# Kernel optimization log

Hardware: AMD Instinct MI355X
Metric: run time of the kernel (lower is better)

The kernel has to match this reference:

```python
import jax, jax.numpy as jnp
import numpy as np

N_NODES = 100000
N_EDGES = 1280000
IN_DIM = 64
OUT_DIM = 64


def setup_inputs() -> dict:
    key = jax.random.key(0)
    k1, k2, k3, k4, k5 = jax.random.split(key, 5)
    features = jax.random.normal(k1, (N_NODES, IN_DIM), dtype=jnp.float32)
    w = jax.random.uniform(k2, (N_EDGES,), dtype=jnp.float32)
    # torch nn.Linear weight is [out, in]; we store it as [in, out] so h @ W
    W = jax.random.normal(k3, (IN_DIM, OUT_DIM), dtype=jnp.float32) * (1.0 / np.sqrt(IN_DIM))
    src = jax.random.randint(k4, (N_EDGES,), 0, N_NODES, dtype=jnp.int64 if jax.config.jax_enable_x64 else jnp.int32)
    dst = jax.random.randint(k5, (N_EDGES,), 0, N_NODES, dtype=jnp.int64 if jax.config.jax_enable_x64 else jnp.int32)
    return {"features": features, "w": w, "W": W, "src": src, "dst": dst}


def reference(features, w, W, src, dst):
    num_nodes = features.shape[0]
    # u_mul_e: per-edge message = h[src] * w  (edge-weighted SpMM gather-multiply)
    msg = features[src] * w[:, None]                     # [E, in_dim]
    # fn.sum('m','h'): scatter-add messages to destination nodes
    agg = jax.ops.segment_sum(msg, dst, num_segments=num_nodes)  # [N, in_dim]
    # D_in = 1 / clamp(in_degree, min=1)
    deg = jax.ops.segment_sum(jnp.ones_like(w), dst, num_segments=num_nodes)
    d_in = 1.0 / jnp.maximum(deg, 1.0)                   # [N]
    h = agg * d_in[:, None]
    # linear (bias=False), activation None, batch_norm False, dropout 0
    return h @ W                                         # [N, out_dim]
```

## Files before the change

kernel.cpp:

```cpp
#include <hip/hip_runtime.h>

#define N_NODES 100000
#define N_EDGES 1280000
#define DIM 64
#define NBINS 391
#define CAP 3712
#define EPB 4096
#define NFB 313
#define CONVB 512
#define NTILES 1563
#define FPAD 68
#define WSCALE (1.0f / 32767.0f)

__device__ __forceinline__ unsigned bf16_rne(float x) {
    unsigned u = __float_as_uint(x);
    return (u + 0x7fffu + ((u >> 16) & 1u)) >> 16;
}
__device__ __forceinline__ float bf_lo(unsigned q) { return __uint_as_float(q << 16); }
__device__ __forceinline__ float bf_hi(unsigned q) { return __uint_as_float(q & 0xffff0000u); }

__global__ __launch_bounds__(256) void k_fill_conv(
    const int* __restrict__ src, const float* __restrict__ w,
    const int* __restrict__ dst, int* __restrict__ cursor,
    uint2* __restrict__ binned,
    const float* __restrict__ feat, const float* __restrict__ W,
    unsigned short* __restrict__ fW) {
    __shared__ union U {
        struct { int h[NBINS]; int base_[NBINS]; } fill;
        struct { float w[DIM * DIM]; float f[64 * FPAD]; } conv;
        __device__ U() {}
    } sm;
    int t = threadIdx.x;

    if (blockIdx.x < NFB) {
        for (int i = t; i < NBINS; i += 256) sm.fill.h[i] = 0;
        __syncthreads();
        int eb = blockIdx.x * EPB;
        int d[16], sv[16];
        unsigned wq[16];
        #pragma unroll
        for (int j = 0; j < 16; ++j) {
            int e = eb + j * 256 + t;
            if (e < N_EDGES) {
                d[j] = dst[e];
                sv[j] = src[e];
                wq[j] = (unsigned)(w[e] * 32767.0f + 0.5f);
                atomicAdd(&sm.fill.h[d[j] >> 8], 1);
            } else d[j] = -1;
        }
        __syncthreads();
        for (int i = t; i < NBINS; i += 256) {
            int c = sm.fill.h[i];
            sm.fill.base_[i] = c ? atomicAdd(&cursor[i], c) : 0;
            sm.fill.h[i] = 0;
        }
        __syncthreads();
        #pragma unroll
        for (int j = 0; j < 16; ++j) {
            if (d[j] >= 0) {
                int bin = d[j] >> 8;
                int pos = sm.fill.base_[bin] + atomicAdd(&sm.fill.h[bin], 1);
                binned[bin * CAP + pos] =
                    make_uint2((unsigned)sv[j] | ((unsigned)(d[j] & 255) << 17), wq[j]);
            }
        }
    } else {
        #pragma unroll
        for (int i = 0; i < DIM * DIM / 256; ++i)
            sm.conv.w[t + i * 256] = W[t + i * 256];
        const float4* lds_w4 = (const float4*)sm.conv.w;
        float4* lds_f4 = (float4*)sm.conv.f;
        int tx = t & 15, ny = t >> 4;
        int rr = t >> 2, seg = t & 3;

        for (int tb = blockIdx.x - NFB; tb < NTILES; tb += CONVB) {
            int nb = tb * 64;
            __syncthreads();
            #pragma unroll
            for (int q = 0; q < 4; ++q) {
                float4 v = (nb + rr < N_NODES)
                           ? ((const float4*)feat)[(size_t)(nb + rr) * 16 + seg * 4 + q]
                           : make_float4(0.f, 0.f, 0.f, 0.f);
                lds_f4[(rr * FPAD + seg * 16 + q * 4) >> 2] = v;
            }
            __syncthreads();
            float acc[4][4];
            #pragma unroll
            for (int i = 0; i < 4; ++i)
                #pragma unroll
                for (int j = 0; j < 4; ++j) acc[i][j] = 0.f;
            for (int k0 = 0; k0 < DIM; k0 += 4) {
                float4 hv[4], wv[4];
                #pragma unroll
                for (int i = 0; i < 4; ++i)
                    hv[i] = lds_f4[((ny * 4 + i) * FPAD + k0) >> 2];
                #pragma unroll
                for (int j = 0; j < 4; ++j)
                    wv[j] = lds_w4[((k0 + j) * DIM + tx * 4) >> 2];
                #pragma unroll
                for (int i = 0; i < 4; ++i) {
                    const float* hp = (const float*)&hv[i];
                    #pragma unroll
                    for (int kk = 0; kk < 4; ++kk) {
                        float hk = hp[kk];
                        acc[i][0] = fmaf(hk, ((const float*)&wv[kk])[0], acc[i][0]);
                        acc[i][1] = fmaf(hk, ((const float*)&wv[kk])[1], acc[i][1]);
                        acc[i][2] = fmaf(hk, ((const float*)&wv[kk])[2], acc[i][2]);
                        acc[i][3] = fmaf(hk, ((const float*)&wv[kk])[3], acc[i][3]);
                    }
                }
            }
            #pragma unroll
            for (int i = 0; i < 4; ++i) {
                int node = nb + ny * 4 + i;
                if (node < N_NODES) {
                    ushort4 o;
                    o.x = (unsigned short)bf16_rne(acc[i][0]);
                    o.y = (unsigned short)bf16_rne(acc[i][1]);
                    o.z = (unsigned short)bf16_rne(acc[i][2]);
                    o.w = (unsigned short)bf16_rne(acc[i][3]);
                    *(ushort4*)(fW + (size_t)node * DIM + tx * 4) = o;
                }
            }
        }
    }
}

__global__ __launch_bounds__(512) void k_sortbin(const uint2* __restrict__ binned,
                                                 const int* __restrict__ cursor,
                                                 unsigned* __restrict__ csrp,
                                                 int* __restrict__ offs,
                                                 int* __restrict__ cnt) {
    __shared__ int h[256];
    __shared__ int excl[256];
    __shared__ unsigned stage[CAP];
    int b = blockIdx.x, t = threadIdx.x;
    int total = cursor[b];
    int segbase = b * CAP;
    if (t < 256) h[t] = 0;
    __syncthreads();
    for (int i = t; i < total; i += 512)
        atomicAdd(&h[(binned[segbase + i].x >> 17) & 255], 1);
    __syncthreads();
    int v = 0;
    if (t < 256) { v = h[t]; excl[t] = v; }
    __syncthreads();
    for (int off = 1; off < 256; off <<= 1) {
        int add = 0;
        if (t < 256 && t >= off) add = excl[t - off];
        __syncthreads();
        if (t < 256) excl[t] += add;
        __syncthreads();
    }
    if (t < 256) {
        int ex = excl[t] - v;
        excl[t] = ex;
        int node = (b << 8) + t;
        if (node < N_NODES) { cnt[node] = v; offs[node] = segbase + ex; }
        h[t] = 0;
    }
    __syncthreads();
    for (int i = t; i < total; i += 512) {
        uint2 e = binned[segbase + i];
        int o = (e.x >> 17) & 255;
        int pos = excl[o] + atomicAdd(&h[o], 1);
        if (pos < CAP) stage[pos] = (e.x & 0x1ffffu) | (e.y << 17);
    }
    __syncthreads();
    for (int i = t; i < total; i += 512)
        csrp[segbase + i] = stage[i];
}

__global__ __launch_bounds__(256) void k_gather(const uint4* __restrict__ fW4,
                                                const unsigned* __restrict__ csrp,
                                                const int* __restrict__ offs,
                                                const int* __restrict__ cnt,
                                                float* __restrict__ out) {
    int lane = threadIdx.x & 63;
    int g = lane >> 3, s = lane & 7;
    int wave = (blockIdx.x * 256 + threadIdx.x) >> 6;
    int nw = gridDim.x * 4;

    for (int node = wave; node < N_NODES; node += nw) {
        int start = offs[node];
        int c = cnt[node];
        int end = start + c;
        float a[8] = {0, 0, 0, 0, 0, 0, 0, 0};
        for (int i = start; i < end; i += 32) {
            int i0 = i + g, i1 = i + 8 + g, i2 = i + 16 + g, i3 = i + 24 + g;
            unsigned p0 = csrp[(i0 < end) ? i0 : start];
            unsigned p1 = csrp[(i1 < end) ? i1 : start];
            unsigned p2 = csrp[(i2 < end) ? i2 : start];
            unsigned p3 = csrp[(i3 < end) ? i3 : start];
            float w0 = (i0 < end) ? (float)(p0 >> 17) * WSCALE : 0.f;
            float w1 = (i1 < end) ? (float)(p1 >> 17) * WSCALE : 0.f;
            float w2 = (i2 < end) ? (float)(p2 >> 17) * WSCALE : 0.f;
            float w3 = (i3 < end) ? (float)(p3 >> 17) * WSCALE : 0.f;
            uint4 q0 = fW4[((p0 & 0x1ffffu) << 3) + s];
            uint4 q1 = fW4[((p1 & 0x1ffffu) << 3) + s];
            uint4 q2 = fW4[((p2 & 0x1ffffu) << 3) + s];
            uint4 q3 = fW4[((p3 & 0x1ffffu) << 3) + s];
            a[0] = fmaf(bf_lo(q0.x), w0, a[0]); a[1] = fmaf(bf_hi(q0.x), w0, a[1]);
            a[2] = fmaf(bf_lo(q0.y), w0, a[2]); a[3] = fmaf(bf_hi(q0.y), w0, a[3]);
            a[4] = fmaf(bf_lo(q0.z), w0, a[4]); a[5] = fmaf(bf_hi(q0.z), w0, a[5]);
            a[6] = fmaf(bf_lo(q0.w), w0, a[6]); a[7] = fmaf(bf_hi(q0.w), w0, a[7]);
            a[0] = fmaf(bf_lo(q1.x), w1, a[0]); a[1] = fmaf(bf_hi(q1.x), w1, a[1]);
            a[2] = fmaf(bf_lo(q1.y), w1, a[2]); a[3] = fmaf(bf_hi(q1.y), w1, a[3]);
            a[4] = fmaf(bf_lo(q1.z), w1, a[4]); a[5] = fmaf(bf_hi(q1.z), w1, a[5]);
            a[6] = fmaf(bf_lo(q1.w), w1, a[6]); a[7] = fmaf(bf_hi(q1.w), w1, a[7]);
            a[0] = fmaf(bf_lo(q2.x), w2, a[0]); a[1] = fmaf(bf_hi(q2.x), w2, a[1]);
            a[2] = fmaf(bf_lo(q2.y), w2, a[2]); a[3] = fmaf(bf_hi(q2.y), w2, a[3]);
            a[4] = fmaf(bf_lo(q2.z), w2, a[4]); a[5] = fmaf(bf_hi(q2.z), w2, a[5]);
            a[6] = fmaf(bf_lo(q2.w), w2, a[6]); a[7] = fmaf(bf_hi(q2.w), w2, a[7]);
            a[0] = fmaf(bf_lo(q3.x), w3, a[0]); a[1] = fmaf(bf_hi(q3.x), w3, a[1]);
            a[2] = fmaf(bf_lo(q3.y), w3, a[2]); a[3] = fmaf(bf_hi(q3.y), w3, a[3]);
            a[4] = fmaf(bf_lo(q3.z), w3, a[4]); a[5] = fmaf(bf_hi(q3.z), w3, a[5]);
            a[6] = fmaf(bf_lo(q3.w), w3, a[6]); a[7] = fmaf(bf_hi(q3.w), w3, a[7]);
        }
        #pragma unroll
        for (int j = 0; j < 8; ++j) {
            a[j] += __shfl_xor(a[j], 8, 64);
            a[j] += __shfl_xor(a[j], 16, 64);
            a[j] += __shfl_xor(a[j], 32, 64);
        }
        float dinv = 1.0f / fmaxf((float)c, 1.0f);
        if (g == 0) {
            float4 o0, o1;
            o0.x = a[0] * dinv; o0.y = a[1] * dinv; o0.z = a[2] * dinv; o0.w = a[3] * dinv;
            o1.x = a[4] * dinv; o1.y = a[5] * dinv; o1.z = a[6] * dinv; o1.w = a[7] * dinv;
            ((float4*)out)[node * 16 + s * 2 + 0] = o0;
            ((float4*)out)[node * 16 + s * 2 + 1] = o1;
        }
    }
}

extern "C" void kernel_launch(void* const* d_in, const int* in_sizes, int n_in,
                              void* d_out, int out_size, void* d_ws, size_t ws_size,
                              hipStream_t stream) {
    const float* feat = (const float*)d_in[0];
    const float* w    = (const float*)d_in[1];
    const float* W    = (const float*)d_in[2];
    const int*   src  = (const int*)d_in[3];
    const int*   dst  = (const int*)d_in[4];
    float* out = (float*)d_out;

    unsigned short* fW = (unsigned short*)d_ws;
    uint2* binned  = (uint2*)(fW + (size_t)N_NODES * DIM);
    unsigned* csrp = (unsigned*)(binned + (size_t)NBINS * CAP);
    int* offs      = (int*)(csrp + (size_t)NBINS * CAP);
    int* cnt       = offs + N_NODES;
    int* cursor    = cnt + N_NODES;

    hipMemsetAsync(cursor, 0, NBINS * sizeof(int), stream);

    k_fill_conv<<<NFB + CONVB, 256, 0, stream>>>(src, w, dst, cursor, binned,
                                                 feat, W, fW);
    k_sortbin<<<NBINS, 512, 0, stream>>>(binned, cursor, csrp, offs, cnt);
    k_gather<<<4096, 256, 0, stream>>>((const uint4*)fW, csrp, offs, cnt, out);
}
```

Measured before the change: 151.4 us.

## Fuse bin sort and gather into one kernel using LDS-staged CSR

Merges the per-bin counting sort and the gather/aggregate pass into one kernel. Each block sorts its bin's edges into shared memory and then gathers directly from that staged CSR, which removes the global csrp/offs/cnt round trip and one launch. Bins shrink from 256 to 128 nodes so a bin fits in LDS and in four edges per thread, and outputs use nontemporal stores. The trade-offs are less gather parallelism per block (8 waves over 128 nodes) and a hard capacity assumption of at most 4 edges per thread and CAP edges per bin.

```diff
diff --git a/kernel.cpp b/kernel.cpp
--- a/kernel.cpp
+++ b/kernel.cpp
@@ -3,14 +3,17 @@
 #define N_NODES 100000
 #define N_EDGES 1280000
 #define DIM 64
-#define NBINS 391
-#define CAP 3712
+#define NBINS 782
+#define BINN 128
+#define CAP 1984
 #define EPB 4096
 #define NFB 313
 #define CONVB 512
 #define NTILES 1563
 #define FPAD 68
 #define WSCALE (1.0f / 32767.0f)
+
+typedef float floatx4 __attribute__((ext_vector_type(4)));
 
 __device__ __forceinline__ unsigned bf16_rne(float x) {
     unsigned u = __float_as_uint(x);
@@ -45,7 +48,7 @@
                 d[j] = dst[e];
                 sv[j] = src[e];
                 wq[j] = (unsigned)(w[e] * 32767.0f + 0.5f);
-                atomicAdd(&sm.fill.h[d[j] >> 8], 1);
+                atomicAdd(&sm.fill.h[d[j] >> 7], 1);
             } else d[j] = -1;
         }
         __syncthreads();
@@ -58,10 +61,10 @@
         #pragma unroll
         for (int j = 0; j < 16; ++j) {
             if (d[j] >= 0) {
-                int bin = d[j] >> 8;
+                int bin = d[j] >> 7;
                 int pos = sm.fill.base_[bin] + atomicAdd(&sm.fill.h[bin], 1);
                 binned[bin * CAP + pos] =
-                    make_uint2((unsigned)sv[j] | ((unsigned)(d[j] & 255) << 17), wq[j]);
+                    make_uint2((unsigned)sv[j] | ((unsigned)(d[j] & 127) << 17), wq[j]);
             }
         }
     } else {
@@ -126,80 +129,75 @@
     }
 }
 
-__global__ __launch_bounds__(512) void k_sortbin(const uint2* __restrict__ binned,
-                                                 const int* __restrict__ cursor,
-                                                 unsigned* __restrict__ csrp,
-                                                 int* __restrict__ offs,
-                                                 int* __restrict__ cnt) {
-    __shared__ int h[256];
-    __shared__ int excl[256];
+__global__ __launch_bounds__(512) void k_sortgather(
+    const uint2* __restrict__ binned, const int* __restrict__ cursor,
+    const uint4* __restrict__ fW4, float* __restrict__ out) {
     __shared__ unsigned stage[CAP];
-    int b = blockIdx.x, t = threadIdx.x;
+    __shared__ int hist[BINN];
+    __shared__ int excl[BINN];
+    __shared__ int hcur[BINN];
+    int t = threadIdx.x, b = blockIdx.x;
     int total = cursor[b];
-    int segbase = b * CAP;
-    if (t < 256) h[t] = 0;
-    __syncthreads();
-    for (int i = t; i < total; i += 512)
-        atomicAdd(&h[(binned[segbase + i].x >> 17) & 255], 1);
+    const uint2* eb = binned + (size_t)b * CAP;
+    if (t < BINN) { hist[t] = 0; hcur[t] = 0; }
+    __syncthreads();
+
+    uint2 ed[4];
+    int ne = 0;
+    for (int i = t; i < total; i += 512) {
+        ed[ne] = eb[i];
+        atomicAdd(&hist[(ed[ne].x >> 17) & 127], 1);
+        ++ne;
+    }
     __syncthreads();
     int v = 0;
-    if (t < 256) { v = h[t]; excl[t] = v; }
-    __syncthreads();
-    for (int off = 1; off < 256; off <<= 1) {
+    if (t < BINN) { v = hist[t]; excl[t] = v; }
+    __syncthreads();
+    #pragma unroll
+    for (int off = 1; off < BINN; off <<= 1) {
         int add = 0;
-        if (t < 256 && t >= off) add = excl[t - off];
-        __syncthreads();
-        if (t < 256) excl[t] += add;
-        __syncthreads();
-    }
-    if (t < 256) {
-        int ex = excl[t] - v;
-        excl[t] = ex;
-        int node = (b << 8) + t;
-        if (node < N_NODES) { cnt[node] = v; offs[node] = segbase + ex; }
-        h[t] = 0;
-    }
-    __syncthreads();
-    for (int i = t; i < total; i += 512) {
-        uint2 e = binned[segbase + i];
-        int o = (e.x >> 17) & 255;
-        int pos = excl[o] + atomicAdd(&h[o], 1);
-        if (pos < CAP) stage[pos] = (e.x & 0x1ffffu) | (e.y << 17);
-    }
-    __syncthreads();
-    for (int i = t; i < total; i += 512)
-        csrp[segbase + i] = stage[i];
-}
-
-__global__ __launch_bounds__(256) void k_gather(const uint4* __restrict__ fW4,
-                                                const unsigned* __restrict__ csrp,
-                                                const int* __restrict__ offs,
-                                                const int* __restrict__ cnt,
-                                                float* __restrict__ out) {
-    int lane = threadIdx.x & 63;
+        if (t < BINN && t >= off) add = excl[t - off];
+        __syncthreads();
+        if (t < BINN) excl[t] += add;
+        __syncthreads();
+    }
+    if (t < BINN) excl[t] -= v;
+    __syncthreads();
+    #pragma unroll
+    for (int k = 0; k < 4; ++k) {
+        if (k < ne) {
+            unsigned x = ed[k].x;
+            int o = (x >> 17) & 127;
+            int pos = excl[o] + atomicAdd(&hcur[o], 1);
+            stage[pos] = (x & 0x1ffffu) | (ed[k].y << 17);
+        }
+    }
+    __syncthreads();
+
+    int lane = t & 63;
+    int wv = t >> 6;
     int g = lane >> 3, s = lane & 7;
-    int wave = (blockIdx.x * 256 + threadIdx.x) >> 6;
-    int nw = gridDim.x * 4;
-
-    for (int node = wave; node < N_NODES; node += nw) {
-        int start = offs[node];
-        int c = cnt[node];
+    for (int n = wv; n < BINN; n += 8) {
+        int node = (b << 7) + n;
+        if (node >= N_NODES) break;
+        int start = excl[n];
+        int c = hist[n];
         int end = start + c;
         float a[8] = {0, 0, 0, 0, 0, 0, 0, 0};
         for (int i = start; i < end; i += 32) {
             int i0 = i + g, i1 = i + 8 + g, i2 = i + 16 + g, i3 = i + 24 + g;
-            unsigned p0 = csrp[(i0 < end) ? i0 : start];
-            unsigned p1 = csrp[(i1 < end) ? i1 : start];
-            unsigned p2 = csrp[(i2 < end) ? i2 : start];
-            unsigned p3 = csrp[(i3 < end) ? i3 : start];
+            unsigned p0 = stage[(i0 < end) ? i0 : start];
+            unsigned p1 = stage[(i1 < end) ? i1 : start];
+            unsigned p2 = stage[(i2 < end) ? i2 : start];
+            unsigned p3 = stage[(i3 < end) ? i3 : start];
             float w0 = (i0 < end) ? (float)(p0 >> 17) * WSCALE : 0.f;
             float w1 = (i1 < end) ? (float)(p1 >> 17) * WSCALE : 0.f;
             float w2 = (i2 < end) ? (float)(p2 >> 17) * WSCALE : 0.f;
             float w3 = (i3 < end) ? (float)(p3 >> 17) * WSCALE : 0.f;
-            uint4 q0 = fW4[((p0 & 0x1ffffu) << 3) + s];
-            uint4 q1 = fW4[((p1 & 0x1ffffu) << 3) + s];
-            uint4 q2 = fW4[((p2 & 0x1ffffu) << 3) + s];
-            uint4 q3 = fW4[((p3 & 0x1ffffu) << 3) + s];
+            uint4 q0 = fW4[((size_t)(p0 & 0x1ffffu) << 3) + s];
+            uint4 q1 = fW4[((size_t)(p1 & 0x1ffffu) << 3) + s];
+            uint4 q2 = fW4[((size_t)(p2 & 0x1ffffu) << 3) + s];
+            uint4 q3 = fW4[((size_t)(p3 & 0x1ffffu) << 3) + s];
             a[0] = fmaf(bf_lo(q0.x), w0, a[0]); a[1] = fmaf(bf_hi(q0.x), w0, a[1]);
             a[2] = fmaf(bf_lo(q0.y), w0, a[2]); a[3] = fmaf(bf_hi(q0.y), w0, a[3]);
             a[4] = fmaf(bf_lo(q0.z), w0, a[4]); a[5] = fmaf(bf_hi(q0.z), w0, a[5]);
@@ -225,11 +223,12 @@
         }
         float dinv = 1.0f / fmaxf((float)c, 1.0f);
         if (g == 0) {
-            float4 o0, o1;
+            floatx4 o0, o1;
             o0.x = a[0] * dinv; o0.y = a[1] * dinv; o0.z = a[2] * dinv; o0.w = a[3] * dinv;
             o1.x = a[4] * dinv; o1.y = a[5] * dinv; o1.z = a[6] * dinv; o1.w = a[7] * dinv;
-            ((float4*)out)[node * 16 + s * 2 + 0] = o0;
-            ((float4*)out)[node * 16 + s * 2 + 1] = o1;
+            floatx4* op = (floatx4*)out + (size_t)node * 16 + s * 2;
+            __builtin_nontemporal_store(o0, op + 0);
+            __builtin_nontemporal_store(o1, op + 1);
         }
     }
 }
@@ -246,15 +245,11 @@
 
     unsigned short* fW = (unsigned short*)d_ws;
     uint2* binned  = (uint2*)(fW + (size_t)N_NODES * DIM);
-    unsigned* csrp = (unsigned*)(binned + (size_t)NBINS * CAP);
-    int* offs      = (int*)(csrp + (size_t)NBINS * CAP);
-    int* cnt       = offs + N_NODES;
-    int* cursor    = cnt + N_NODES;
+    int* cursor    = (int*)(binned + (size_t)NBINS * CAP);
 
     hipMemsetAsync(cursor, 0, NBINS * sizeof(int), stream);
 
     k_fill_conv<<<NFB + CONVB, 256, 0, stream>>>(src, w, dst, cursor, binned,
                                                  feat, W, fW);
-    k_sortbin<<<NBINS, 512, 0, stream>>>(binned, cursor, csrp, offs, cnt);
-    k_gather<<<4096, 256, 0, stream>>>((const uint4*)fW, csrp, offs, cnt, out);
-}
+    k_sortgather<<<NBINS, 512, 0, stream>>>(binned, cursor, (const uint4*)fW, out);
+}
```

New measurement: 182.8 us. 1.21x slower.

## Process two nodes per wavefront in gather, pack offset/count, use nontemporal loads/stores

Applied to the files above, without the earlier changes.

The gather kernel now gives each half-wave (32 lanes) its own destination node, so one wave handles two nodes at once and walks 16 edges per iteration instead of 32. This cuts the lanes idling on masked edges for low-degree nodes (average degree about 13) and drops one shuffle-reduction stage. Offsets and counts are packed into a single int2 array, so each node needs one load instead of two. Edge-list reads and output writes use nontemporal hints to keep them from polluting the cache used for feature rows. As a side effect, per-node loop trip counts can now diverge between the two halves of a wave.

```diff
diff --git a/kernel.cpp b/kernel.cpp
--- a/kernel.cpp
+++ b/kernel.cpp
@@ -11,6 +11,8 @@
 #define NTILES 1563
 #define FPAD 68
 #define WSCALE (1.0f / 32767.0f)
+
+typedef float floatx4 __attribute__((ext_vector_type(4)));
 
 __device__ __forceinline__ unsigned bf16_rne(float x) {
     unsigned u = __float_as_uint(x);
@@ -129,8 +131,7 @@
 __global__ __launch_bounds__(512) void k_sortbin(const uint2* __restrict__ binned,
                                                  const int* __restrict__ cursor,
                                                  unsigned* __restrict__ csrp,
-                                                 int* __restrict__ offs,
-                                                 int* __restrict__ cnt) {
+                                                 int2* __restrict__ noff) {
     __shared__ int h[256];
     __shared__ int excl[256];
     __shared__ unsigned stage[CAP];
@@ -156,7 +157,7 @@
         int ex = excl[t] - v;
         excl[t] = ex;
         int node = (b << 8) + t;
-        if (node < N_NODES) { cnt[node] = v; offs[node] = segbase + ex; }
+        if (node < N_NODES) noff[node] = make_int2(segbase + ex, v);
         h[t] = 0;
     }
     __syncthreads();
@@ -173,33 +174,35 @@
 
 __global__ __launch_bounds__(256) void k_gather(const uint4* __restrict__ fW4,
                                                 const unsigned* __restrict__ csrp,
-                                                const int* __restrict__ offs,
-                                                const int* __restrict__ cnt,
+                                                const int2* __restrict__ noff,
                                                 float* __restrict__ out) {
     int lane = threadIdx.x & 63;
-    int g = lane >> 3, s = lane & 7;
+    int h = lane >> 5;
+    int g2 = (lane >> 3) & 3;
+    int s = lane & 7;
     int wave = (blockIdx.x * 256 + threadIdx.x) >> 6;
     int nw = gridDim.x * 4;
 
-    for (int node = wave; node < N_NODES; node += nw) {
-        int start = offs[node];
-        int c = cnt[node];
+    for (int pair = wave; pair < N_NODES / 2; pair += nw) {
+        int node = pair * 2 + h;
+        int2 oc = noff[node];
+        int start = oc.x, c = oc.y;
         int end = start + c;
         float a[8] = {0, 0, 0, 0, 0, 0, 0, 0};
-        for (int i = start; i < end; i += 32) {
-            int i0 = i + g, i1 = i + 8 + g, i2 = i + 16 + g, i3 = i + 24 + g;
-            unsigned p0 = csrp[(i0 < end) ? i0 : start];
-            unsigned p1 = csrp[(i1 < end) ? i1 : start];
-            unsigned p2 = csrp[(i2 < end) ? i2 : start];
-            unsigned p3 = csrp[(i3 < end) ? i3 : start];
+        for (int i = start; i < end; i += 16) {
+            int i0 = i + g2, i1 = i + 4 + g2, i2 = i + 8 + g2, i3 = i + 12 + g2;
+            unsigned p0 = __builtin_nontemporal_load(csrp + ((i0 < end) ? i0 : start));
+            unsigned p1 = __builtin_nontemporal_load(csrp + ((i1 < end) ? i1 : start));
+            unsigned p2 = __builtin_nontemporal_load(csrp + ((i2 < end) ? i2 : start));
+            unsigned p3 = __builtin_nontemporal_load(csrp + ((i3 < end) ? i3 : start));
             float w0 = (i0 < end) ? (float)(p0 >> 17) * WSCALE : 0.f;
             float w1 = (i1 < end) ? (float)(p1 >> 17) * WSCALE : 0.f;
             float w2 = (i2 < end) ? (float)(p2 >> 17) * WSCALE : 0.f;
             float w3 = (i3 < end) ? (float)(p3 >> 17) * WSCALE : 0.f;
-            uint4 q0 = fW4[((p0 & 0x1ffffu) << 3) + s];
-            uint4 q1 = fW4[((p1 & 0x1ffffu) << 3) + s];
-            uint4 q2 = fW4[((p2 & 0x1ffffu) << 3) + s];
-            uint4 q3 = fW4[((p3 & 0x1ffffu) << 3) + s];
+            uint4 q0 = fW4[((size_t)(p0 & 0x1ffffu) << 3) + s];
+            uint4 q1 = fW4[((size_t)(p1 & 0x1ffffu) << 3) + s];
+            uint4 q2 = fW4[((size_t)(p2 & 0x1ffffu) << 3) + s];
+            uint4 q3 = fW4[((size_t)(p3 & 0x1ffffu) << 3) + s];
             a[0] = fmaf(bf_lo(q0.x), w0, a[0]); a[1] = fmaf(bf_hi(q0.x), w0, a[1]);
             a[2] = fmaf(bf_lo(q0.y), w0, a[2]); a[3] = fmaf(bf_hi(q0.y), w0, a[3]);
             a[4] = fmaf(bf_lo(q0.z), w0, a[4]); a[5] = fmaf(bf_hi(q0.z), w0, a[5]);
@@ -221,15 +224,15 @@
         for (int j = 0; j < 8; ++j) {
             a[j] += __shfl_xor(a[j], 8, 64);
             a[j] += __shfl_xor(a[j], 16, 64);
-            a[j] += __shfl_xor(a[j], 32, 64);
         }
         float dinv = 1.0f / fmaxf((float)c, 1.0f);
-        if (g == 0) {
-            float4 o0, o1;
+        if (g2 == 0) {
+            floatx4 o0, o1;
             o0.x = a[0] * dinv; o0.y = a[1] * dinv; o0.z = a[2] * dinv; o0.w = a[3] * dinv;
             o1.x = a[4] * dinv; o1.y = a[5] * dinv; o1.z = a[6] * dinv; o1.w = a[7] * dinv;
-            ((float4*)out)[node * 16 + s * 2 + 0] = o0;
-            ((float4*)out)[node * 16 + s * 2 + 1] = o1;
+            floatx4* op = (floatx4*)out + (size_t)node * 16 + s * 2;
+            __builtin_nontemporal_store(o0, op + 0);
+            __builtin_nontemporal_store(o1, op + 1);
         }
     }
 }
@@ -247,14 +250,13 @@
     unsigned short* fW = (unsigned short*)d_ws;
     uint2* binned  = (uint2*)(fW + (size_t)N_NODES * DIM);
     unsigned* csrp = (unsigned*)(binned + (size_t)NBINS * CAP);
-    int* offs      = (int*)(csrp + (size_t)NBINS * CAP);
-    int* cnt       = offs + N_NODES;
-    int* cursor    = cnt + N_NODES;
+    int2* noff     = (int2*)(csrp + (size_t)NBINS * CAP);
+    int* cursor    = (int*)(noff + N_NODES);
 
     hipMemsetAsync(cursor, 0, NBINS * sizeof(int), stream);
 
     k_fill_conv<<<NFB + CONVB, 256, 0, stream>>>(src, w, dst, cursor, binned,
                                                  feat, W, fW);
-    k_sortbin<<<NBINS, 512, 0, stream>>>(binned, cursor, csrp, offs, cnt);
-    k_gather<<<4096, 256, 0, stream>>>((const uint4*)fW, csrp, offs, cnt, out);
-}
+    k_sortbin<<<NBINS, 512, 0, stream>>>(binned, cursor, csrp, noff);
+    k_gather<<<4096, 256, 0, stream>>>((const uint4*)fW, csrp, noff, out);
+}
```

After: 142.9 us. 5.6% less time.
